# Performance work log

Hardware: AMD Instinct MI355X
Metric: run time of the kernel (lower is better)

The kernel has to match this reference:

```python
import jax, jax.numpy as jnp
import numpy as np

V = 4096   # vocal_size
M = 4      # markov_order
B = 8
L = 2048


def setup_inputs() -> dict:
    key = jax.random.key(0)
    k1, k2 = jax.random.split(key, 2)
    idx = jax.random.randint(k1, (B, L), 0, V, dtype=jnp.int64 if jax.config.jax_enable_x64 else jnp.int32)
    fan_in = M * (V + 1)
    # nn.Linear default init: U(-1/sqrt(fan_in), 1/sqrt(fan_in))
    bound = 1.0 / np.sqrt(fan_in)
    W = jax.random.uniform(k2, (V, fan_in), minval=-bound, maxval=bound, dtype=jnp.float32)
    b = jax.random.uniform(jax.random.fold_in(k2, 1), (V,), minval=-bound, maxval=bound, dtype=jnp.float32)
    return {"idx": idx, "W": W, "b": b}


def _contexts(idx, vocab, order):
    # Reproduces the roll-and-pad loop: x[..., k] = idx shifted right by (order-1-k),
    # with the first (order-1-k) positions filled with the pad token `vocab`.
    Bb, Ll = idx.shape
    cols = []
    for k in range(order):
        s = order - 1 - k
        if s == 0:
            cols.append(idx)
        else:
            pad = jnp.full((Bb, s), vocab, dtype=idx.dtype)
            cols.append(jnp.concatenate([pad, idx[:, : Ll - s]], axis=1))
    return jnp.stack(cols, axis=-1)  # [B, L, M]


def reference(idx, W, b):
    vocab = W.shape[0]
    order = W.shape[1] // (vocab + 1)
    x = _contexts(idx, vocab, order)          # [B, L, M]
    # one_hot(x) @ W.T == gather rows of W.T per table; split W.T into M tables.
    Wt = W.T.reshape(order, vocab + 1, vocab)  # [M, V+1, V]
    logits = b
    for k in range(order):  # small fixed loop over markov order
        logits = logits + Wt[k][x[..., k]]     # [B, L, V]
    return logits
```

## Files before the change

kernel.cpp:

```cpp
#include <hip/hip_runtime.h>
#include <hip/hip_bf16.h>
#include <cstdint>

#define VOCAB 4096
#define ORDER 4
#define FAN   16388
#define NL    2048
#define NPOS  16384

typedef float        f4 __attribute__((ext_vector_type(4)));
typedef unsigned int u4 __attribute__((ext_vector_type(4)));
typedef unsigned int u2 __attribute__((ext_vector_type(2)));

static __device__ __forceinline__ unsigned short f2bf(float f)
{
    __hip_bfloat16 h = __float2bfloat16(f);
    unsigned short r;
    __builtin_memcpy(&r, &h, 2);
    return r;
}

__global__ __launch_bounds__(512) void k_transpose_bf16(
    const float* __restrict__ W, unsigned short* __restrict__ Wt)
{
    __shared__ float tile[128][129];
    const int c0 = blockIdx.x * 128;
    const int v0 = blockIdx.y * 128;

    const int cq = (threadIdx.x & 31) * 4;
    const int vr = threadIdx.x >> 5;
    const bool cvalid = (c0 + cq) < FAN;

    #pragma unroll
    for (int i = 0; i < 8; ++i) {
        const int v = vr + 16 * i;
        if (cvalid) {
            const f4 f = __builtin_nontemporal_load(
                (const f4*)(W + (size_t)(v0 + v) * FAN + (c0 + cq)));
            tile[v][cq + 0] = f.x;
            tile[v][cq + 1] = f.y;
            tile[v][cq + 2] = f.z;
            tile[v][cq + 3] = f.w;
        }
    }
    __syncthreads();

    const int p  = (threadIdx.x & 15) * 8;
    const int cb = threadIdx.x >> 4;

    #pragma unroll
    for (int i = 0; i < 4; ++i) {
        const int cl = cb + 32 * i;
        const int c  = c0 + cl;
        if (c < FAN) {
            unsigned short s[8];
            #pragma unroll
            for (int j = 0; j < 8; ++j)
                s[j] = f2bf(tile[p + j][cl]);
            u4 pk;
            pk.x = (unsigned)s[0] | ((unsigned)s[1] << 16);
            pk.y = (unsigned)s[2] | ((unsigned)s[3] << 16);
            pk.z = (unsigned)s[4] | ((unsigned)s[5] << 16);
            pk.w = (unsigned)s[6] | ((unsigned)s[7] << 16);
            *(u4*)(Wt + (size_t)c * VOCAB + v0 + p) = pk;
        }
    }
}

__device__ __forceinline__ void accum4(float* acc, const u2& a)
{
    acc[0] += __uint_as_float(a.x << 16);
    acc[1] += __uint_as_float(a.x & 0xFFFF0000u);
    acc[2] += __uint_as_float(a.y << 16);
    acc[3] += __uint_as_float(a.y & 0xFFFF0000u);
}

__global__ __launch_bounds__(256) void k_gather(
    const int* __restrict__ idx, const unsigned short* __restrict__ Wt,
    const float* __restrict__ bias, float* __restrict__ out)
{
    const int pp = blockIdx.x * 2;
    const int bb = pp >> 11;
    const int l0 = pp & (NL - 1);
    const int* row = idx + bb * NL;

    const unsigned short* r[2][ORDER];
    #pragma unroll
    for (int k = 0; k < ORDER; ++k) {
        const int s  = ORDER - 1 - k;
        const int t0 = (l0 >= s)     ? row[l0 - s]     : VOCAB;
        const int t1 = (l0 + 1 >= s) ? row[l0 + 1 - s] : VOCAB;
        r[0][k] = Wt + (size_t)(k * (VOCAB + 1) + t0) * VOCAB;
        r[1][k] = Wt + (size_t)(k * (VOCAB + 1) + t1) * VOCAB;
    }

    float* o0 = out + (size_t)pp * VOCAB;
    float* o1 = o0 + VOCAB;
    const int j4 = threadIdx.x * 4;

    #pragma unroll
    for (int seg = 0; seg < 4; ++seg) {
        const int v = seg * 1024 + j4;

        const f4 b = *(const f4*)(bias + v);
        float a0[4] = {b.x, b.y, b.z, b.w};
        float a1[4] = {b.x, b.y, b.z, b.w};

        #pragma unroll
        for (int k = 0; k < ORDER; ++k) {
            const u2 w0 = *(const u2*)(r[0][k] + v);
            const u2 w1 = *(const u2*)(r[1][k] + v);
            accum4(a0, w0);
            accum4(a1, w1);
        }

        f4 s0; s0.x = a0[0]; s0.y = a0[1]; s0.z = a0[2]; s0.w = a0[3];
        f4 s1; s1.x = a1[0]; s1.y = a1[1]; s1.z = a1[2]; s1.w = a1[3];
        __builtin_nontemporal_store(s0, (f4*)(o0 + v));
        __builtin_nontemporal_store(s1, (f4*)(o1 + v));
    }
}

__global__ __launch_bounds__(256) void k_direct(
    const int* __restrict__ idx, const float* __restrict__ W,
    const float* __restrict__ bias, float* __restrict__ out)
{
    const int pos = blockIdx.x;
    const int bb  = pos >> 11;
    const int ll  = pos & (NL - 1);
    const int* row = idx + bb * NL;

    int off[ORDER];
    #pragma unroll
    for (int k = 0; k < ORDER; ++k) {
        const int s   = ORDER - 1 - k;
        const int tok = (ll >= s) ? row[ll - s] : VOCAB;
        off[k] = k * (VOCAB + 1) + tok;
    }

    float* o = out + (size_t)pos * VOCAB;
    for (int v = threadIdx.x; v < VOCAB; v += 256) {
        const float* wr = W + (size_t)v * FAN;
        o[v] = bias[v] + wr[off[0]] + wr[off[1]] + wr[off[2]] + wr[off[3]];
    }
}

extern "C" void kernel_launch(void* const* d_in, const int* in_sizes, int n_in,
                              void* d_out, int out_size, void* d_ws, size_t ws_size,
                              hipStream_t stream)
{
    const int*   idx  = (const int*)d_in[0];
    const float* W    = (const float*)d_in[1];
    const float* bias = (const float*)d_in[2];
    float*       out  = (float*)d_out;

    const size_t wt_bytes = (size_t)FAN * VOCAB * 2;

    if (ws_size >= wt_bytes) {
        unsigned short* Wt = (unsigned short*)d_ws;
        dim3 g1((FAN + 127) / 128, VOCAB / 128);
        k_transpose_bf16<<<g1, 512, 0, stream>>>(W, Wt);
        k_gather<<<NPOS / 2, 256, 0, stream>>>(idx, Wt, bias, out);
    } else {
        k_direct<<<NPOS, 256, 0, stream>>>(idx, W, bias, out);
    }
}
```

Before: 507.9 us.

## Pipeline W transpose via async global-to-LDS loads and gather four positions per block

Replaces the one-tile-per-block transpose with a persistent 256-block kernel that double-buffers 128x128 tiles in 128 KiB of dynamic LDS. Tiles are loaded with global_load_lds and an XOR swizzle, and the next tile's load overlaps the current tile's bf16 conversion and store. The gather kernel now handles four positions per block with 32-bit byte offsets and issues all row loads before accumulating, to raise memory-level parallelism. The changes risk low occupancy from the large LDS footprint and depend on the hand-written vmcnt wait being correct.

```diff
diff --git a/kernel.cpp b/kernel.cpp
--- a/kernel.cpp
+++ b/kernel.cpp
@@ -7,6 +7,7 @@
 #define FAN   16388
 #define NL    2048
 #define NPOS  16384
+#define NCT   129
 
 typedef float        f4 __attribute__((ext_vector_type(4)));
 typedef unsigned int u4 __attribute__((ext_vector_type(4)));
@@ -18,6 +19,86 @@
     unsigned short r;
     __builtin_memcpy(&r, &h, 2);
     return r;
+}
+
+__global__ __launch_bounds__(512) void k_transpose_pipe(
+    const float* __restrict__ W, unsigned short* __restrict__ Wt)
+{
+    extern __shared__ float buf[];
+
+    const int b   = blockIdx.x;
+    const int vt  = b & 31;
+    const int g   = b >> 5;
+    const int ct0 = (g * NCT) / 8;
+    const int ct1 = ((g + 1) * NCT) / 8;
+    const int v0  = vt * 128;
+
+    const int tid  = threadIdx.x;
+    const int lane = tid & 63;
+    const int w    = tid >> 6;
+
+    const int lrow_half = lane >> 5;
+    const int lgran     = lane & 31;
+
+    const int pth = (tid & 15) * 8;
+    const int cb  = tid >> 4;
+    const int sth = (tid & 15) & 7;
+
+    int cur = 0;
+
+    auto stage = [&](int ct, int pg) {
+        const int c0 = ct * 128;
+        #pragma unroll
+        for (int i = 0; i < 8; ++i) {
+            const int r = w * 16 + 2 * i + lrow_half;
+            const int s = (r >> 3) & 7;
+            int c = c0 + 4 * (lgran ^ s);
+            if (c + 4 > FAN) c = c0;
+            const float* gp = W + (size_t)(v0 + r) * FAN + c;
+            float* lp = buf + pg * 16384 + (w * 16 + 2 * i) * 128;
+            __builtin_amdgcn_global_load_lds(
+                (const __attribute__((address_space(1))) unsigned int*)gp,
+                (__attribute__((address_space(3))) unsigned int*)lp,
+                16, 0, 2 );
+        }
+    };
+
+    auto store_phase = [&](int ct, int pg) {
+        const int c0 = ct * 128;
+        const float* bp = buf + pg * 16384;
+        #pragma unroll
+        for (int i = 0; i < 4; ++i) {
+            const int cl = cb + 32 * i;
+            const int c  = c0 + cl;
+            if (c < FAN) {
+                const int gsw = (((cl >> 2) ^ sth) << 2) + (cl & 3);
+                unsigned short sv[8];
+                #pragma unroll
+                for (int j = 0; j < 8; ++j)
+                    sv[j] = f2bf(bp[(pth + j) * 128 + gsw]);
+                u4 pk;
+                pk.x = (unsigned)sv[0] | ((unsigned)sv[1] << 16);
+                pk.y = (unsigned)sv[2] | ((unsigned)sv[3] << 16);
+                pk.z = (unsigned)sv[4] | ((unsigned)sv[5] << 16);
+                pk.w = (unsigned)sv[6] | ((unsigned)sv[7] << 16);
+                *(u4*)(Wt + (size_t)c * VOCAB + v0 + pth) = pk;
+            }
+        }
+    };
+
+    stage(ct0, 0);
+    __syncthreads();
+
+    for (int t = ct0; t < ct1; ++t) {
+        const bool more = (t + 1 < ct1);
+        if (more) stage(t + 1, cur ^ 1);
+        store_phase(t, cur);
+        if (more) {
+            asm volatile("s_waitcnt vmcnt(4)" ::: "memory");
+            __builtin_amdgcn_s_barrier();
+        }
+        cur ^= 1;
+    }
 }
 
 __global__ __launch_bounds__(512) void k_transpose_bf16(
@@ -67,57 +148,59 @@
     }
 }
 
-__device__ __forceinline__ void accum4(float* acc, const u2& a)
-{
-    acc[0] += __uint_as_float(a.x << 16);
-    acc[1] += __uint_as_float(a.x & 0xFFFF0000u);
-    acc[2] += __uint_as_float(a.y << 16);
-    acc[3] += __uint_as_float(a.y & 0xFFFF0000u);
-}
-
-__global__ __launch_bounds__(256) void k_gather(
+__global__ __launch_bounds__(256) void k_gather4(
     const int* __restrict__ idx, const unsigned short* __restrict__ Wt,
     const float* __restrict__ bias, float* __restrict__ out)
 {
-    const int pp = blockIdx.x * 2;
+    const int pp = blockIdx.x * 4;
     const int bb = pp >> 11;
     const int l0 = pp & (NL - 1);
     const int* row = idx + bb * NL;
 
-    const unsigned short* r[2][ORDER];
-    #pragma unroll
-    for (int k = 0; k < ORDER; ++k) {
-        const int s  = ORDER - 1 - k;
-        const int t0 = (l0 >= s)     ? row[l0 - s]     : VOCAB;
-        const int t1 = (l0 + 1 >= s) ? row[l0 + 1 - s] : VOCAB;
-        r[0][k] = Wt + (size_t)(k * (VOCAB + 1) + t0) * VOCAB;
-        r[1][k] = Wt + (size_t)(k * (VOCAB + 1) + t1) * VOCAB;
-    }
-
-    float* o0 = out + (size_t)pp * VOCAB;
-    float* o1 = o0 + VOCAB;
+    unsigned off[4][ORDER];
+    #pragma unroll
+    for (int p = 0; p < 4; ++p) {
+        #pragma unroll
+        for (int k = 0; k < ORDER; ++k) {
+            const int s   = ORDER - 1 - k;
+            const int lp  = l0 + p;
+            const int tok = (lp >= s) ? row[lp - s] : VOCAB;
+            off[p][k] = (unsigned)(((size_t)(k * (VOCAB + 1) + tok) * VOCAB) * 2u);
+        }
+    }
+
+    const char* Wb = (const char*)Wt;
+    float* o = out + (size_t)pp * VOCAB;
     const int j4 = threadIdx.x * 4;
 
     #pragma unroll
     for (int seg = 0; seg < 4; ++seg) {
-        const int v = seg * 1024 + j4;
-
-        const f4 b = *(const f4*)(bias + v);
-        float a0[4] = {b.x, b.y, b.z, b.w};
-        float a1[4] = {b.x, b.y, b.z, b.w};
-
-        #pragma unroll
-        for (int k = 0; k < ORDER; ++k) {
-            const u2 w0 = *(const u2*)(r[0][k] + v);
-            const u2 w1 = *(const u2*)(r[1][k] + v);
-            accum4(a0, w0);
-            accum4(a1, w1);
-        }
-
-        f4 s0; s0.x = a0[0]; s0.y = a0[1]; s0.z = a0[2]; s0.w = a0[3];
-        f4 s1; s1.x = a1[0]; s1.y = a1[1]; s1.z = a1[2]; s1.w = a1[3];
-        __builtin_nontemporal_store(s0, (f4*)(o0 + v));
-        __builtin_nontemporal_store(s1, (f4*)(o1 + v));
+        const int v    = seg * 1024 + j4;
+        const int voff = v * 2;
+
+        const f4 bv = *(const f4*)(bias + v);
+
+        u2 wv[4][ORDER];
+        #pragma unroll
+        for (int p = 0; p < 4; ++p)
+            #pragma unroll
+            for (int k = 0; k < ORDER; ++k)
+                wv[p][k] = *(const u2*)(Wb + off[p][k] + voff);
+
+        #pragma unroll
+        for (int p = 0; p < 4; ++p) {
+            float a0 = bv.x, a1 = bv.y, a2 = bv.z, a3 = bv.w;
+            #pragma unroll
+            for (int k = 0; k < ORDER; ++k) {
+                const unsigned lo = wv[p][k].x, hi = wv[p][k].y;
+                a0 += __uint_as_float(lo << 16);
+                a1 += __uint_as_float(lo & 0xFFFF0000u);
+                a2 += __uint_as_float(hi << 16);
+                a3 += __uint_as_float(hi & 0xFFFF0000u);
+            }
+            f4 sv; sv.x = a0; sv.y = a1; sv.z = a2; sv.w = a3;
+            __builtin_nontemporal_store(sv, (f4*)(o + (size_t)p * VOCAB + v));
+        }
     }
 }
 
@@ -158,9 +241,22 @@
 
     if (ws_size >= wt_bytes) {
         unsigned short* Wt = (unsigned short*)d_ws;
-        dim3 g1((FAN + 127) / 128, VOCAB / 128);
-        k_transpose_bf16<<<g1, 512, 0, stream>>>(W, Wt);
-        k_gather<<<NPOS / 2, 256, 0, stream>>>(idx, Wt, bias, out);
+
+        static int pipe_ok = -1;
+        if (pipe_ok < 0) {
+            pipe_ok = (hipFuncSetAttribute(
+                           (const void*)k_transpose_pipe,
+                           hipFuncAttributeMaxDynamicSharedMemorySize,
+                           131072) == hipSuccess) ? 1 : 0;
+        }
+
+        if (pipe_ok) {
+            k_transpose_pipe<<<256, 512, 131072, stream>>>(W, Wt);
+        } else {
+            dim3 g1((FAN + 127) / 128, VOCAB / 128);
+            k_transpose_bf16<<<g1, 512, 0, stream>>>(W, Wt);
+        }
+        k_gather4<<<NPOS / 4, 256, 0, stream>>>(idx, Wt, bias, out);
     } else {
         k_direct<<<NPOS, 256, 0, stream>>>(idx, W, bias, out);
     }
```

After: 513.8 us. No clear change (+1.2%).
